# Kernel tuning notes

Hardware: AMD Instinct MI355X
Metric: run time of the kernel (lower is better)

The kernel has to match this reference:

```python
import jax, jax.numpy as jnp
import numpy as np

SR = 2            # search_range
LEAK = 0.2        # keras.activations.leaky_relu default negative_slope


def _conv(x, k, b):
    y = jax.lax.conv_general_dilated(x, k, (1, 1), 'SAME',
                                     dimension_numbers=('NHWC', 'HWIO', 'NHWC'))
    return y + b


def _lrelu(x):
    return jnp.where(x >= 0, x, LEAK * x)


def _bilinear_sample(imgs, cx, cy):
    # Faithful to the keras BilinearSampler: indices are PIXEL-flat (b*H*W + y*W + x)
    # but keras.ops.take flattens imgs over ALL dims (incl. channels), so the gather
    # reads from imgs.reshape(-1) at those pixel-flat positions and output has 1 channel.
    B, H, W, C = imgs.shape
    x0 = jnp.floor(cx); x1 = x0 + 1.0
    y0 = jnp.floor(cy); y1 = y0 + 1.0
    wt_x0 = x1 - cx; wt_x1 = cx - x0
    wt_y0 = y1 - cy; wt_y1 = cy - y0
    x_max = float(W - 1); y_max = float(H - 1)
    x0s = jnp.clip(x0, 0.0, x_max); x1s = jnp.clip(x1, 0.0, x_max)
    y0s = jnp.clip(y0, 0.0, y_max); y1s = jnp.clip(y1, 0.0, y_max)
    dim2 = float(W)
    base = (jnp.arange(B, dtype=jnp.float32) * float(H * W)).reshape(B, 1, 1, 1)
    by0 = base + y0s * dim2
    by1 = base + y1s * dim2
    flat = imgs.reshape(-1)
    g = lambda idx: jnp.take(flat, idx.astype(jnp.int32))
    im00 = g(x0s + by0); im01 = g(x0s + by1)
    im10 = g(x1s + by0); im11 = g(x1s + by1)
    return (wt_x0 * wt_y0) * im00 + (wt_x0 * wt_y1) * im01 \
         + (wt_x1 * wt_y0) * im10 + (wt_x1 * wt_y1) * im11


def _module_m(left, right, prev_disp, params):
    B, H, W, C = left.shape
    # upsample previous disparity to this level's resolution (bilinear, half-pixel)
    up = jax.image.resize(prev_disp, (B, H, W, 1), method='bilinear')
    # build sampling coords: x = j - flow, y = i (flow y-component is zeros)
    jj = jnp.arange(W, dtype=jnp.float32).reshape(1, 1, W, 1)
    ii = jnp.arange(H, dtype=jnp.float32).reshape(1, H, 1, 1)
    cx = jj - up                                   # [B,H,W,1]
    cy = jnp.broadcast_to(ii, (B, H, W, 1))        # [B,H,W,1]
    warped = _bilinear_sample(right, cx, cy)       # [B,H,W,1]
    # cost volume: shifted products, channel-mean (warped broadcasts over C)
    padded = jnp.pad(warped, ((0, 0), (0, 0), (SR, SR), (0, 0)))
    costs = [jnp.mean(left * padded[:, :, i:W + i, :], axis=3, keepdims=True)
             for i in range(2 * SR + 1)]
    cost_curve = jnp.concatenate([left] + costs, axis=-1)   # [B,H,W,C+5]
    vol = jnp.concatenate([cost_curve, up], axis=-1)        # [B,H,W,C+6]
    x = _lrelu(_conv(vol, params['k1'], params['b1']))
    x = _lrelu(_conv(x, params['k2'], params['b2']))
    x = _lrelu(_conv(x, params['k3'], params['b3']))
    x = _lrelu(_conv(x, params['k4'], params['b4']))
    x = _lrelu(_conv(x, params['k5'], params['b5']))
    x = _conv(x, params['k6'], params['b6'])                # linear head -> [B,H,W,1]
    return x


def setup_inputs() -> dict:
    key = jax.random.key(0)
    ks = jax.random.split(key, 16)
    B, H, W, C = 8, 128, 256, 128
    left = jax.random.normal(ks[0], (B, H, W, C), dtype=jnp.float32)
    right = jax.random.normal(ks[1], (B, H, W, C), dtype=jnp.float32)
    prev_disp = jax.random.uniform(ks[2], (B, H // 2, W // 2, 1), dtype=jnp.float32) * 8.0
    in_ch = C + (2 * SR + 1) + 1  # 134
    chans = [(in_ch, 128), (128, 128), (128, 96), (96, 64), (64, 32), (32, 1)]
    inp = {'left': left, 'right': right, 'prev_disp': prev_disp}
    for i, (ci, co) in enumerate(chans, start=1):
        inp[f'k{i}'] = jax.random.normal(ks[2 + 2 * i], (3, 3, ci, co), dtype=jnp.float32) * 0.05
        inp[f'b{i}'] = jnp.zeros((co,), dtype=jnp.float32)
    return inp


def reference(left, right, prev_disp, k1, b1, k2, b2, k3, b3, k4, b4, k5, b5, k6, b6):
    params = {'k1': k1, 'b1': b1, 'k2': k2, 'b2': b2, 'k3': k3, 'b3': b3,
              'k4': k4, 'b4': b4, 'k5': k5, 'b5': b5, 'k6': k6, 'b6': b6}
    return _module_m(left, right, prev_disp, params)
```

## Files before the change

### kernel.cpp

```cpp
#include <hip/hip_runtime.h>

typedef __attribute__((ext_vector_type(8))) short short8;
typedef __attribute__((ext_vector_type(4))) float f32x4;
typedef __attribute__((ext_vector_type(4))) unsigned short us4;

#define LEAK 0.2f

__device__ __forceinline__ float b2f(unsigned short s) {
    unsigned u = ((unsigned)s) << 16;
    return __builtin_bit_cast(float, u);
}
__device__ __forceinline__ unsigned short f2b(float f) {
    unsigned u = __builtin_bit_cast(unsigned, f);
    u += 0x7fffu + ((u >> 16) & 1u);
    return (unsigned short)(u >> 16);
}

__device__ __forceinline__ void async16(const short* g, short* l) {
    __builtin_amdgcn_global_load_lds(
        (const __attribute__((address_space(1))) void*)g,
        (__attribute__((address_space(3))) void*)l, 16, 0, 0);
}

__global__ __launch_bounds__(256)
void prep_kernel(const float* __restrict__ left, const float* __restrict__ right,
                 const float* __restrict__ pd, short* __restrict__ vol) {
    __shared__ __align__(16) float inL[64 * 132];
    __shared__ __align__(16) float rrow[256];
    __shared__ __align__(16) float pr0[128];
    __shared__ __align__(16) float pr1[128];
    __shared__ __align__(16) short outT[64 * 144];

    int t = threadIdx.x;
    int blk = blockIdx.x;
    int wq = blk & 3, h = (blk >> 2) & 127, b = blk >> 9;
    int w0 = wq << 6;

    float sy = h * 0.5f - 0.25f;
    float fy0 = floorf(sy);
    float fy = sy - fy0;
    int y0 = (int)fy0;
    int y0c = min(max(y0, 0), 63), y1c = min(max(y0 + 1, 0), 63);

    const float* lp = left + ((size_t)((b * 128 + h) * 256 + w0)) * 128;
#pragma unroll
    for (int k2 = 0; k2 < 8; ++k2) {
        int g = t + k2 * 256;
        int p = g >> 5, j = g & 31;
        float4 v = *(const float4*)(lp + (size_t)g * 4);
        *(float4*)(&inL[p * 132 + j * 4]) = v;
    }
    if (t < 64) {
        *(float4*)(&rrow[t * 4]) =
            *(const float4*)(right + ((size_t)(b * 128 + h)) * 256 + t * 4);
    } else if (t < 96) {
        int i2 = t - 64;
        *(float4*)(&pr0[i2 * 4]) = *(const float4*)(pd + (size_t)(b * 64 + y0c) * 128 + i2 * 4);
    } else if (t < 128) {
        int i2 = t - 96;
        *(float4*)(&pr1[i2 * 4]) = *(const float4*)(pd + (size_t)(b * 64 + y1c) * 128 + i2 * 4);
    }
    __syncthreads();

    int p = t >> 2, s = t & 3;
    int w = w0 + p;
    const float* src = &inL[p * 132 + s * 32];
    short* odst = &outT[p * 144 + s * 32];
    float sum = 0.f;
#pragma unroll
    for (int i = 0; i < 8; ++i) {
        float f0 = src[i * 4], f1 = src[i * 4 + 1], f2 = src[i * 4 + 2], f3 = src[i * 4 + 3];
        sum += (f0 + f1) + (f2 + f3);
        us4 o;
        o.x = f2b(f0); o.y = f2b(f1); o.z = f2b(f2); o.w = f2b(f3);
        *(us4*)(odst + i * 4) = o;
    }
    sum += __shfl_xor(sum, 1);
    sum += __shfl_xor(sum, 2);
    float mean = sum * (1.f / 128.f);

    float one_fy = 1.f - fy;
#pragma unroll
    for (int tap = s; tap < 5; tap += 4) {
        int jj = w + tap - 2;
        if (jj >= 0 && jj < 256) {
            float sx = jj * 0.5f - 0.25f;
            float fx0 = floorf(sx);
            float fx = sx - fx0;
            int x0 = (int)fx0;
            int x0c = min(max(x0, 0), 127), x1c = min(max(x0 + 1, 0), 127);
            float up = one_fy * ((1.f - fx) * pr0[x0c] + fx * pr0[x1c])
                     + fy     * ((1.f - fx) * pr1[x0c] + fx * pr1[x1c]);
            float cx = (float)jj - up;
            float xf0 = floorf(cx), xf1 = xf0 + 1.f;
            float w0x = xf1 - cx, w1x = cx - xf0;
            int ix0 = (int)fminf(fmaxf(xf0, 0.f), 255.f);
            int ix1 = (int)fminf(fmaxf(xf1, 0.f), 255.f);
            float warped = w0x * rrow[ix0] + w1x * rrow[ix1];
            outT[p * 144 + 128 + tap] = (short)f2b(warped * mean);
            if (tap == 2) outT[p * 144 + 133] = (short)f2b(up);
        } else {
            outT[p * 144 + 128 + tap] = 0;
        }
    }
    if (s == 0) { outT[p * 144 + 134] = 0; outT[p * 144 + 135] = 0; }
    if (s == 3) {
        us4 z = {};
        *(us4*)(&outT[p * 144 + 136]) = z;
        *(us4*)(&outT[p * 144 + 140]) = z;
    }
    __syncthreads();

    short* gdst = vol + ((size_t)(b * 130 + h + 1) * 258 + (w0 + 1)) * 144;
    for (int g = t; g < 1152; g += 256)
        *(short8*)(gdst + g * 8) = *(const short8*)(&outT[g * 8]);
}

__global__ void halo_zero_one(short* __restrict__ buf, int C) {
    int nchunk = C >> 3;
    int slot = blockIdx.x * 256 + threadIdx.x;
    int total = 8 * 772 * nchunk;
    if (slot >= total) return;
    int chunk = slot % nchunk;
    int pix = slot / nchunk;
    int b = pix / 772, p = pix % 772;
    int row, col;
    if (p < 516) { row = (p < 258) ? 0 : 129; col = (p < 258) ? p : p - 258; }
    else { int q = p - 516; row = 1 + (q >> 1); col = (q & 1) ? 257 : 0; }
    short8 z = {};
    *(short8*)(buf + ((size_t)(b * 130 + row) * 258 + col) * C + chunk * 8) = z;
}

__global__ void wconv_all(const float* __restrict__ k1, const float* __restrict__ k2,
                          const float* __restrict__ k3, const float* __restrict__ k4,
                          const float* __restrict__ k5,
                          short* __restrict__ w1, short* __restrict__ w2,
                          short* __restrict__ w3, short* __restrict__ w4,
                          short* __restrict__ w5) {
    const int CINt[5]  = {134, 128, 128, 96, 64};
    const int COUTt[5] = {128, 128, 96, 64, 32};
    const int KCt[5]   = {5, 4, 4, 3, 2};
    const float* srcs[5] = {k1, k2, k3, k4, k5};
    short* dsts[5] = {w1, w2, w3, w4, w5};
    int l = blockIdx.y;
    int CIN = CINt[l], COUT = COUTt[l], KC = KCt[l];
    const float* k = srcs[l];
    short* wt = dsts[l];
    int idx = blockIdx.x * 256 + threadIdx.x;
    int total = 9 * KC * COUT * 32;
    if (idx >= total) return;
    int j = idx & 7;
    int s = (idx >> 3) & 3;
    int rest = idx >> 5;
    int n = rest % COUT; rest /= COUT;
    int tap = rest % 9, kc = rest / 9;
    int q = (s - (n >> 1)) & 3;
    int kk = q * 8 + j;
    int ci = kc * 32 + kk;
    float v = (ci < CIN) ? k[(size_t)(tap * CIN + ci) * COUT + n] : 0.f;
    wt[idx] = (short)f2b(v);
}

template <int KC, int CIN_STR, int COUT, int NT, int LASTC>
__launch_bounds__(512, 2)
__global__ void conv3x3_kernel(const short* __restrict__ in, const short* __restrict__ wt,
                               const float* __restrict__ bias, short* __restrict__ out) {
    __shared__ short ldsA[2][10 * 66 * 4 * 8];
    __shared__ short ldsW[9 * COUT * 32];
    const int WSLOTS = 9 * COUT * 4;
    const int WSTRIDE = 9 * COUT * 32;

    int t = threadIdx.x;
    int lane = t & 63, wid = t >> 6;
    int q = lane >> 4, col = lane & 15;
    int out_row = wid;

    int wtile = blockIdx.x & 3;
    int rest = blockIdx.x >> 2;
    int htile = rest & 15, b = rest >> 4;
    int w0h = wtile << 6;
    int row0 = htile << 3;

    const short* inbase = in + ((size_t)(b * 130 + row0) * 258 + w0h) * CIN_STR;

    auto stageA = [&](int kc, int d) {
        short* dst = &ldsA[d][0];
        for (int i = t; i < 2640; i += 512) {
            int r = i / 264, rem = i % 264;
            int p = rem >> 2, s = rem & 3;
            int c = (s - (p >> 1)) & 3;
            if (LASTC == 4 || kc < KC - 1 || c < LASTC) {
                const short* g = inbase + ((size_t)r * 258 + p) * CIN_STR + kc * 32 + c * 8;
                async16(g, dst + (size_t)(i & ~63) * 8);
            }
        }
    };
    auto stageW = [&](int kc) {
        const short* wsrc = wt + (size_t)kc * WSTRIDE;
        for (int i = t; i < WSLOTS; i += 512)
            async16(wsrc + (size_t)i * 8, ldsW + (size_t)(i & ~63) * 8);
    };

    f32x4 acc[4][NT] = {};

    stageW(0);
    stageA(0, 0);
    __syncthreads();

    for (int kc = 0; kc < KC; ++kc) {
        if (kc + 1 < KC) stageA(kc + 1, (kc + 1) & 1);
        const short* A = &ldsA[kc & 1][0];

#pragma unroll
        for (int dy = 0; dy < 3; ++dy) {
            int ldsrow = out_row + dy;
#pragma unroll
            for (int dx = 0; dx < 3; ++dx) {
                short8 a[4], bfr[NT];
#pragma unroll
                for (int mt = 0; mt < 4; ++mt) {
                    int p = mt * 16 + col + dx;
                    a[mt] = *(const short8*)(A +
                        (size_t)(((ldsrow * 66 + p) << 2) + ((q + (p >> 1)) & 3)) * 8);
                }
                const short* wp = ldsW + (size_t)(dy * 3 + dx) * COUT * 32;
#pragma unroll
                for (int nt = 0; nt < NT; ++nt) {
                    int n = nt * 16 + col;
                    bfr[nt] = *(const short8*)(wp +
                        (size_t)((n << 2) + ((q + (n >> 1)) & 3)) * 8);
                }
#pragma unroll
                for (int mt = 0; mt < 4; ++mt)
#pragma unroll
                    for (int nt = 0; nt < NT; ++nt)
                        acc[mt][nt] = __builtin_amdgcn_mfma_f32_16x16x32_bf16(
                            a[mt], bfr[nt], acc[mt][nt], 0, 0, 0);
            }
        }
        __syncthreads();
        if (kc + 1 < KC) {
            stageW(kc + 1);
            __syncthreads();
        }
    }

    size_t obase = ((size_t)(b * 130 + row0 + 1 + out_row) * 258 + (w0h + 1)) * COUT;
#pragma unroll
    for (int nt = 0; nt < NT; ++nt) {
        int n = nt * 16 + col;
        float bv = bias[n];
#pragma unroll
        for (int mt = 0; mt < 4; ++mt) {
#pragma unroll
            for (int rr = 0; rr < 4; ++rr) {
                int m = mt * 16 + q * 4 + rr;
                float v = acc[mt][nt][rr] + bv;
                v = (v >= 0.f) ? v : LEAK * v;
                out[obase + (size_t)m * COUT + n] = (short)f2b(v);
            }
        }
    }
}

__global__ void conv6_kernel(const short* __restrict__ x, const float* __restrict__ k,
                             const float* __restrict__ bias, float* __restrict__ out) {
    __shared__ float wk[288];
    int t = threadIdx.x;
    for (int i = t; i < 288; i += 256) wk[i] = k[i];
    __syncthreads();
    int idx = blockIdx.x * 256 + t;
    int w = idx & 255, h = (idx >> 8) & 127, b = idx >> 15;
    float acc = bias[0];
#pragma unroll
    for (int dy = 0; dy < 3; ++dy) {
#pragma unroll
        for (int dx = 0; dx < 3; ++dx) {
            const short* xp = x + ((size_t)(b * 130 + h + dy) * 258 + (w + dx)) * 32;
            const float* wp = wk + (dy * 3 + dx) * 32;
#pragma unroll
            for (int c8 = 0; c8 < 4; ++c8) {
                short8 v = *(const short8*)(xp + c8 * 8);
#pragma unroll
                for (int j = 0; j < 8; ++j)
                    acc += b2f((unsigned short)v[j]) * wp[c8 * 8 + j];
            }
        }
    }
    out[idx] = acc;
}

extern "C" void kernel_launch(void* const* d_in, const int* in_sizes, int n_in,
                              void* d_out, int out_size, void* d_ws, size_t ws_size,
                              hipStream_t stream) {
    const float* left  = (const float*)d_in[0];
    const float* right = (const float*)d_in[1];
    const float* pd    = (const float*)d_in[2];
    const float* k[6];
    const float* bb[6];
    for (int i = 0; i < 6; ++i) { k[i] = (const float*)d_in[3 + 2 * i]; bb[i] = (const float*)d_in[4 + 2 * i]; }

    char* ws = (char*)d_ws;
    short* wt1 = (short*)ws;
    short* wt2 = (short*)(ws + 368640);
    short* wt3 = (short*)(ws + 663552);
    short* wt4 = (short*)(ws + 884736);
    short* wt5 = (short*)(ws + 995328);
    short* vol = (short*)(ws + 1048576);
    short* X1  = (short*)(ws + 1048576 + 77276160);
    short* X2  = vol;
    short* X3  = X1;
    short* X4  = vol;
    short* X5  = X1;

    auto hz = [&](short* buf, int C) {
        int blocks = (8 * 772 * (C >> 3) + 255) / 256;
        halo_zero_one<<<blocks, 256, 0, stream>>>(buf, C);
    };

    prep_kernel<<<4096, 256, 0, stream>>>(left, right, pd, vol);
    wconv_all<<<dim3(720, 5), 256, 0, stream>>>(k[0], k[1], k[2], k[3], k[4],
                                                wt1, wt2, wt3, wt4, wt5);
    hz(vol, 144);
    hz(X1, 128);

    conv3x3_kernel<5, 144, 128, 8, 2><<<512, 512, 0, stream>>>(vol, wt1, bb[0], X1);
    hz(X2, 128);
    conv3x3_kernel<4, 128, 128, 8, 4><<<512, 512, 0, stream>>>(X1, wt2, bb[1], X2);
    hz(X3, 96);
    conv3x3_kernel<4, 128,  96, 6, 4><<<512, 512, 0, stream>>>(X2, wt3, bb[2], X3);
    hz(X4, 64);
    conv3x3_kernel<3,  96,  64, 4, 4><<<512, 512, 0, stream>>>(X3, wt4, bb[3], X4);
    hz(X5, 32);
    conv3x3_kernel<2,  64,  32, 2, 4><<<512, 512, 0, stream>>>(X4, wt5, bb[4], X5);
    conv6_kernel<<<1024, 256, 0, stream>>>(X5, k[5], bb[5], (float*)d_out);
}
```

Baseline: 604.8 us.

## Restructure conv LDS layouts with padded strides and per-row weight double buffering

Replaces the XOR-swizzled LDS layouts for activations and weights with channel-chunk-major layouts padded by one element (67 pixels, COUT+1), so fragment loads become simple constant-offset addressing. Weights are now staged per (kc, dy) phase into a double-buffered LDS slice instead of a full 9-tap slab, which shrinks LDS use and overlaps the weight load with compute. Staging offsets are precomputed per thread so no division runs inside the loop. In exchange there is one barrier per dy instead of per kc, and padding may leave some LDS bank conflicts if the stride choice is imperfect.

```diff
diff --git a/kernel.cpp b/kernel.cpp
--- a/kernel.cpp
+++ b/kernel.cpp
@@ -146,18 +146,20 @@
     int CIN = CINt[l], COUT = COUTt[l], KC = KCt[l];
     const float* k = srcs[l];
     short* wt = dsts[l];
+    int WS = 4 * 3 * (COUT + 1);
+    int total = KC * 3 * WS * 8;
     int idx = blockIdx.x * 256 + threadIdx.x;
-    int total = 9 * KC * COUT * 32;
     if (idx >= total) return;
     int j = idx & 7;
-    int s = (idx >> 3) & 3;
-    int rest = idx >> 5;
-    int n = rest % COUT; rest /= COUT;
-    int tap = rest % 9, kc = rest / 9;
-    int q = (s - (n >> 1)) & 3;
-    int kk = q * 8 + j;
-    int ci = kc * 32 + kk;
-    float v = (ci < CIN) ? k[(size_t)(tap * CIN + ci) * COUT + n] : 0.f;
+    int g = idx >> 3;
+    int ph = g / WS, gs = g % WS;
+    int kc = ph / 3, dy = ph % 3;
+    int n = gs % (COUT + 1);
+    int g2 = gs / (COUT + 1);
+    int dx = g2 % 3, qq = g2 / 3;
+    int tap = dy * 3 + dx;
+    int ci = kc * 32 + qq * 8 + j;
+    float v = (n < COUT && ci < CIN) ? k[(size_t)(tap * CIN + ci) * COUT + n] : 0.f;
     wt[idx] = (short)f2b(v);
 }
 
@@ -165,15 +167,14 @@
 __launch_bounds__(512, 2)
 __global__ void conv3x3_kernel(const short* __restrict__ in, const short* __restrict__ wt,
                                const float* __restrict__ bias, short* __restrict__ out) {
-    __shared__ short ldsA[2][10 * 66 * 4 * 8];
-    __shared__ short ldsW[9 * COUT * 32];
-    const int WSLOTS = 9 * COUT * 4;
-    const int WSTRIDE = 9 * COUT * 32;
+    const int AG = 4 * 10 * 67;
+    const int WS = 4 * 3 * (COUT + 1);
+    __shared__ short ldsA[2][AG * 8];
+    __shared__ short ldsW[2][WS * 8];
 
     int t = threadIdx.x;
     int lane = t & 63, wid = t >> 6;
     int q = lane >> 4, col = lane & 15;
-    int out_row = wid;
 
     int wtile = blockIdx.x & 3;
     int rest = blockIdx.x >> 2;
@@ -183,53 +184,64 @@
 
     const short* inbase = in + ((size_t)(b * 130 + row0) * 258 + w0h) * CIN_STR;
 
+    int agoff[6], ac[6], avalid[6];
+#pragma unroll
+    for (int s = 0; s < 6; ++s) {
+        int i = t + s * 512;
+        int c = i / 670, rem = i % 670;
+        int row = rem / 67, p = rem % 67;
+        ac[s] = c;
+        avalid[s] = (i < AG) && (p < 66);
+        agoff[s] = (row * 258 + p) * CIN_STR + c * 8;
+    }
+    int ldst0 = (t & ~63) * 8;
+
     auto stageA = [&](int kc, int d) {
-        short* dst = &ldsA[d][0];
-        for (int i = t; i < 2640; i += 512) {
-            int r = i / 264, rem = i % 264;
-            int p = rem >> 2, s = rem & 3;
-            int c = (s - (p >> 1)) & 3;
-            if (LASTC == 4 || kc < KC - 1 || c < LASTC) {
-                const short* g = inbase + ((size_t)r * 258 + p) * CIN_STR + kc * 32 + c * 8;
-                async16(g, dst + (size_t)(i & ~63) * 8);
-            }
+        short* dst = &ldsA[d][ldst0];
+#pragma unroll
+        for (int s = 0; s < 6; ++s) {
+            if (avalid[s] && (LASTC == 4 || kc < KC - 1 || ac[s] < LASTC))
+                async16(inbase + agoff[s] + kc * 32, dst + s * 512 * 8);
         }
     };
-    auto stageW = [&](int kc) {
-        const short* wsrc = wt + (size_t)kc * WSTRIDE;
-        for (int i = t; i < WSLOTS; i += 512)
-            async16(wsrc + (size_t)i * 8, ldsW + (size_t)(i & ~63) * 8);
+    auto stageW = [&](int ph, int d) {
+        const short* src = wt + (size_t)ph * WS * 8;
+        short* dst = &ldsW[d][ldst0];
+#pragma unroll
+        for (int s = 0; s < (WS + 511) / 512; ++s) {
+            int i = t + s * 512;
+            if (i < WS) async16(src + (size_t)i * 8, dst + s * 512 * 8);
+        }
     };
 
     f32x4 acc[4][NT] = {};
 
-    stageW(0);
     stageA(0, 0);
+    stageW(0, 0);
     __syncthreads();
 
+    int aoff = ((q * 10 + wid) * 67 + col) * 16;
+    int woff = (q * 3 * (COUT + 1) + col) * 16;
+
+    int wb = 0;
     for (int kc = 0; kc < KC; ++kc) {
-        if (kc + 1 < KC) stageA(kc + 1, (kc + 1) & 1);
-        const short* A = &ldsA[kc & 1][0];
-
+        const char* Acur = (const char*)&ldsA[kc & 1][0] + aoff;
 #pragma unroll
         for (int dy = 0; dy < 3; ++dy) {
-            int ldsrow = out_row + dy;
+            int ph = kc * 3 + dy;
+            if (ph + 1 < 3 * KC) stageW(ph + 1, wb ^ 1);
+            if (dy == 0 && kc + 1 < KC) stageA(kc + 1, (kc + 1) & 1);
+            const char* ab = Acur + dy * 1072;
+            const char* wp = (const char*)&ldsW[wb][0] + woff;
 #pragma unroll
             for (int dx = 0; dx < 3; ++dx) {
                 short8 a[4], bfr[NT];
 #pragma unroll
-                for (int mt = 0; mt < 4; ++mt) {
-                    int p = mt * 16 + col + dx;
-                    a[mt] = *(const short8*)(A +
-                        (size_t)(((ldsrow * 66 + p) << 2) + ((q + (p >> 1)) & 3)) * 8);
-                }
-                const short* wp = ldsW + (size_t)(dy * 3 + dx) * COUT * 32;
-#pragma unroll
-                for (int nt = 0; nt < NT; ++nt) {
-                    int n = nt * 16 + col;
-                    bfr[nt] = *(const short8*)(wp +
-                        (size_t)((n << 2) + ((q + (n >> 1)) & 3)) * 8);
-                }
+                for (int mt = 0; mt < 4; ++mt)
+                    a[mt] = *(const short8*)(ab + dx * 16 + mt * 256);
+#pragma unroll
+                for (int nt = 0; nt < NT; ++nt)
+                    bfr[nt] = *(const short8*)(wp + dx * (COUT + 1) * 16 + nt * 256);
 #pragma unroll
                 for (int mt = 0; mt < 4; ++mt)
 #pragma unroll
@@ -237,15 +249,12 @@
                         acc[mt][nt] = __builtin_amdgcn_mfma_f32_16x16x32_bf16(
                             a[mt], bfr[nt], acc[mt][nt], 0, 0, 0);
             }
-        }
-        __syncthreads();
-        if (kc + 1 < KC) {
-            stageW(kc + 1);
             __syncthreads();
-        }
-    }
-
-    size_t obase = ((size_t)(b * 130 + row0 + 1 + out_row) * 258 + (w0h + 1)) * COUT;
+            wb ^= 1;
+        }
+    }
+
+    size_t obase = ((size_t)(b * 130 + row0 + 1 + wid) * 258 + (w0h + 1)) * COUT;
 #pragma unroll
     for (int nt = 0; nt < NT; ++nt) {
         int n = nt * 16 + col;
@@ -302,10 +311,10 @@
 
     char* ws = (char*)d_ws;
     short* wt1 = (short*)ws;
-    short* wt2 = (short*)(ws + 368640);
-    short* wt3 = (short*)(ws + 663552);
-    short* wt4 = (short*)(ws + 884736);
-    short* wt5 = (short*)(ws + 995328);
+    short* wt2 = (short*)(ws + 371520);
+    short* wt3 = (short*)(ws + 668736);
+    short* wt4 = (short*)(ws + 892224);
+    short* wt5 = (short*)(ws + 1004544);
     short* vol = (short*)(ws + 1048576);
     short* X1  = (short*)(ws + 1048576 + 77276160);
     short* X2  = vol;
@@ -319,7 +328,7 @@
     };
 
     prep_kernel<<<4096, 256, 0, stream>>>(left, right, pd, vol);
-    wconv_all<<<dim3(720, 5), 256, 0, stream>>>(k[0], k[1], k[2], k[3], k[4],
+    wconv_all<<<dim3(726, 5), 256, 0, stream>>>(k[0], k[1], k[2], k[3], k[4],
                                                 wt1, wt2, wt3, wt4, wt5);
     hz(vol, 144);
     hz(X1, 128);
```

Measured after the change: 670.4 us. +10.8%, slower.
